# Kernel tuning notes

Measured on AMD Instinct MI355X. Metric: run time of the kernel, lower is better.

The kernel has to match this reference:

```python
import jax, jax.numpy as jnp
import numpy as np

HEADS = 16
HEAD_DIM = 64
DIM = 1024
INNER = HEADS * HEAD_DIM
EPS = 1e-5


def setup_inputs() -> dict:
    key = jax.random.key(0)
    k_x, k_qkv, k_out, k_b = jax.random.split(key, 4)
    B, L = 2, 2048
    x = jax.random.normal(k_x, (B, L, DIM), dtype=jnp.float32)
    # Linear weights stored as [in, out] for x @ W
    w_qkv = jax.random.normal(k_qkv, (DIM, 3 * INNER), dtype=jnp.float32) * (DIM ** -0.5)
    w_out = jax.random.normal(k_out, (INNER, DIM), dtype=jnp.float32) * (INNER ** -0.5)
    b_out = jax.random.normal(k_b, (DIM,), dtype=jnp.float32) * 0.02
    gamma = jnp.ones((DIM,), dtype=jnp.float32)
    beta = jnp.zeros((DIM,), dtype=jnp.float32)
    return {"x": x, "w_qkv": w_qkv, "w_out": w_out, "b_out": b_out, "gamma": gamma, "beta": beta}


def reference(x, w_qkv, w_out, b_out, gamma, beta):
    B, L, C = x.shape
    scale = HEAD_DIM ** -0.5
    qkv = x @ w_qkv  # [B, L, 3*INNER]
    q, k, v = jnp.split(qkv, 3, axis=-1)
    # [B, L, INNER] -> [B, H, L, D]
    def split_heads(t):
        return t.reshape(B, L, HEADS, HEAD_DIM).transpose(0, 2, 1, 3)
    q, k, v = split_heads(q), split_heads(k), split_heads(v)
    dots = jnp.einsum('bhid,bhjd->bhij', q, k) * scale
    attn = jax.nn.softmax(dots, axis=-1)
    out = jnp.einsum('bhij,bhjd->bhid', attn, v)
    out = out.transpose(0, 2, 1, 3).reshape(B, L, INNER)
    out = out @ w_out + b_out
    res = x + out
    mean = jnp.mean(res, axis=-1, keepdims=True)
    var = jnp.var(res, axis=-1, keepdims=True)
    return (res - mean) * jax.lax.rsqrt(var + EPS) * gamma + beta
```

## Files before the change

### kernel.cpp

```cpp
#include <hip/hip_runtime.h>
#include <hip/hip_bf16.h>
#include <stdint.h>

#define HEADS 16
#define HDIM  64
#define DIMC  1024
#define INNER 1024
#define LSEQ  2048
#define BLM   4096

typedef unsigned short u16;
typedef __attribute__((ext_vector_type(8))) short bf16x8;
typedef __attribute__((ext_vector_type(4))) float f32x4;

__device__ __forceinline__ u16 f2bf(float f) {
  union { float f; uint32_t u; } v; v.f = f;
  uint32_t u = v.u;
  return (u16)((u + 0x7fffu + ((u >> 16) & 1u)) >> 16);
}
__device__ __forceinline__ uint32_t pack_bf2(float a, float b) {
  float2 f2; f2.x = a; f2.y = b;
  __hip_bfloat162 t = __float22bfloat162_rn(f2);
  union { __hip_bfloat162 h; uint32_t u; } c; c.h = t; return c.u;
}
__device__ __forceinline__ float fast_exp2(float x) {
  float r; asm("v_exp_f32 %0, %1" : "=v"(r) : "v"(x)); return r;
}

__device__ __forceinline__ void load_lds16(const void* g, void* l) {
  __builtin_amdgcn_global_load_lds(
      (const __attribute__((address_space(1))) uint32_t*)g,
      (__attribute__((address_space(3))) uint32_t*)l, 16, 0, 0);
}

__global__ __launch_bounds__(256) void cast_bf16_k(const float* __restrict__ in,
                                                   u16* __restrict__ out, int n) {
  int i = (blockIdx.x * 256 + threadIdx.x) * 4;
  if (i < n) {
    float4 v = *(const float4*)(in + i);
    ushort4 o;
    o.x = f2bf(v.x); o.y = f2bf(v.y); o.z = f2bf(v.z); o.w = f2bf(v.w);
    *(ushort4*)(out + i) = o;
  }
}

__global__ __launch_bounds__(256) void transpose_cast_k(const float* __restrict__ in,
                                                        u16* __restrict__ out,
                                                        int R, int C) {
  __shared__ float tile[32][33];
  int c0 = blockIdx.x * 32, r0 = blockIdx.y * 32;
  int j = threadIdx.x & 31, i0 = threadIdx.x >> 5;
#pragma unroll
  for (int p = 0; p < 4; ++p) {
    int i = i0 + p * 8;
    tile[i][j] = in[(size_t)(r0 + i) * C + (c0 + j)];
  }
  __syncthreads();
#pragma unroll
  for (int p = 0; p < 4; ++p) {
    int i = i0 + p * 8;
    out[(size_t)(c0 + i) * R + (r0 + j)] = f2bf(tile[j][i]);
  }
}

template <int EPI, int TM>
__global__ __launch_bounds__(256) void gemm_bt(const u16* __restrict__ A,
                                               const u16* __restrict__ Bt,
                                               u16* __restrict__ Cb,
                                               float* __restrict__ Cf,
                                               const float* __restrict__ bias,
                                               const float* __restrict__ resid,
                                               u16* __restrict__ Vt,
                                               int M, int N, int K) {
  constexpr int MI = TM / 32;
  __shared__ alignas(16) u16 As[TM * 64];
  __shared__ alignas(16) u16 Bs[128 * 64];
  const int tid = threadIdx.x;
  const int lane = tid & 63;
  const int w = tid >> 6;
  const int wm = w >> 1, wn = w & 1;
  const int m0 = blockIdx.y * TM, n0 = blockIdx.x * 128;
  const int ln = lane & 15, qq = lane >> 4;
  const f32x4 zero4 = {0.f, 0.f, 0.f, 0.f};

  f32x4 acc[MI][4];
#pragma unroll
  for (int i = 0; i < MI; ++i)
#pragma unroll
    for (int j = 0; j < 4; ++j) acc[i][j] = zero4;

  for (int kt = 0; kt < K; kt += 64) {
    __syncthreads();
#pragma unroll
    for (int p = 0; p < TM / 32; ++p) {
      int t = p * 256 + tid;
      int r = t >> 3;
      int cl = (t & 7) ^ (r & 7);
      load_lds16(A + (size_t)(m0 + r) * K + kt + cl * 8,
                 (char*)As + (p * 256 + w * 64) * 16);
    }
#pragma unroll
    for (int p = 0; p < 4; ++p) {
      int t = p * 256 + tid;
      int r = t >> 3;
      int cl = (t & 7) ^ (r & 7);
      load_lds16(Bt + (size_t)(n0 + r) * K + kt + cl * 8,
                 (char*)Bs + (p * 256 + w * 64) * 16);
    }
    __syncthreads();
#pragma unroll
    for (int ks = 0; ks < 2; ++ks) {
      bf16x8 af[MI], bfr[4];
#pragma unroll
      for (int i = 0; i < MI; ++i) {
        int ra = wm * (TM / 2) + i * 16 + ln;
        af[i] = *(const bf16x8*)(As + (ra * 8 + ((ks * 4 + qq) ^ (ra & 7))) * 8);
      }
#pragma unroll
      for (int j = 0; j < 4; ++j) {
        int rb = wn * 64 + j * 16 + ln;
        bfr[j] = *(const bf16x8*)(Bs + (rb * 8 + ((ks * 4 + qq) ^ (rb & 7))) * 8);
      }
#pragma unroll
      for (int i = 0; i < MI; ++i)
#pragma unroll
        for (int j = 0; j < 4; ++j)
          acc[i][j] = __builtin_amdgcn_mfma_f32_16x16x32_bf16(af[i], bfr[j],
                                                              acc[i][j], 0, 0, 0);
    }
  }

#pragma unroll
  for (int i = 0; i < MI; ++i) {
#pragma unroll
    for (int j = 0; j < 4; ++j) {
      int col = n0 + wn * 64 + j * 16 + ln;
      if (EPI == 1) {
#pragma unroll
        for (int rr = 0; rr < 4; ++rr) {
          int row = m0 + wm * (TM / 2) + i * 16 + qq * 4 + rr;
          Cf[(size_t)row * N + col] =
              acc[i][j][rr] + bias[col] + resid[(size_t)row * N + col];
        }
      } else {
        if (col < 2048) {
#pragma unroll
          for (int rr = 0; rr < 4; ++rr) {
            int row = m0 + wm * (TM / 2) + i * 16 + qq * 4 + rr;
            Cb[(size_t)row * 2048 + col] = f2bf(acc[i][j][rr]);
          }
        } else {
          int dg = col - 2048;
          int hh = dg >> 6, dd = dg & 63;
          int l0 = (m0 & 2047) + wm * (TM / 2) + i * 16 + qq * 4;
          int bb = m0 >> 11;
          ushort4 pk;
          pk.x = f2bf(acc[i][j][0]); pk.y = f2bf(acc[i][j][1]);
          pk.z = f2bf(acc[i][j][2]); pk.w = f2bf(acc[i][j][3]);
          *(ushort4*)(Vt + (((size_t)bb * 16 + hh) * 64 + dd) * 2048 + l0) = pk;
        }
      }
    }
  }
}

__global__ __launch_bounds__(256) void attn_fused(const u16* __restrict__ qk,
                                                  const u16* __restrict__ vt,
                                                  u16* __restrict__ outp) {
  const int bh = blockIdx.x & 31;
  const int qt = blockIdx.x >> 5;
  const int h = bh & 15;
  const int b = bh >> 4;
  const int tid = threadIdx.x;
  const int lane = tid & 63;
  const int w = tid >> 6;
  const int ln = lane & 15, q4 = lane >> 4;
  const int l7 = ln & 7;
  const f32x4 zero4 = {0.f, 0.f, 0.f, 0.f};

  __shared__ alignas(16) u16 Ks[64 * 64];
  __shared__ alignas(16) u16 Vs[64 * 64];
  __shared__ alignas(16) u16 Ps[4][16 * 72];

  const size_t bh_tok = (size_t)b * LSEQ;
  const size_t vbase = ((size_t)b * 16 + h) * 64 * 2048;
  const int baseQ = h * HDIM;

  const float qscale = 0.125f * 1.44269504088896340736f;
  bf16x8 qf[2];
  {
    int row = qt * 64 + w * 16 + ln;
    const u16* p = qk + (bh_tok + row) * 2048 + baseQ;
#pragma unroll
    for (int ks = 0; ks < 2; ++ks) {
      bf16x8 v = *(const bf16x8*)(p + q4 * 8 + 32 * ks);
      bf16x8 o;
#pragma unroll
      for (int jj = 0; jj < 8; ++jj) {
        union { uint32_t u; float f; } cv; cv.u = ((uint32_t)(u16)v[jj]) << 16;
        o[jj] = (short)f2bf(cv.f * qscale);
      }
      qf[ks] = o;
    }
  }

  float lsum = 0.f;
  f32x4 o_acc[4];
#pragma unroll
  for (int dt = 0; dt < 4; ++dt) o_acc[dt] = zero4;

  u16* pw_base = &Ps[w][0];

  for (int jt = 0; jt < 32; ++jt) {
    const int key0 = jt * 64;
    __syncthreads();
#pragma unroll
    for (int iss = 0; iss < 2; ++iss) {
      int idx = iss * 256 + tid;
      int row = idx >> 3, c = idx & 7;
      int cl = c ^ (row & 7);
      load_lds16(qk + (bh_tok + key0 + row) * 2048 + 1024 + baseQ + cl * 8,
                 (char*)Ks + (iss * 256 + w * 64) * 16);
      load_lds16(vt + vbase + (size_t)row * 2048 + key0 + cl * 8,
                 (char*)Vs + (iss * 256 + w * 64) * 16);
    }
    __syncthreads();

    f32x4 S[4];
#pragma unroll
    for (int kt = 0; kt < 4; ++kt) {
      f32x4 a = zero4;
#pragma unroll
      for (int ks = 0; ks < 2; ++ks) {
        bf16x8 kf = *(const bf16x8*)(
            Ks + (((kt * 16 + ln) * 8 + ((ks * 4 + q4) ^ l7)) * 8));
        a = __builtin_amdgcn_mfma_f32_16x16x32_bf16(kf, qf[ks], a, 0, 0, 0);
      }
      S[kt] = a;
    }

#pragma unroll
    for (int kt = 0; kt < 4; ++kt)
#pragma unroll
      for (int r = 0; r < 4; ++r) {
        float p = fast_exp2(S[kt][r]);
        S[kt][r] = p;
        lsum += p;
      }

#pragma unroll
    for (int kt = 0; kt < 4; ++kt) {
      uint2 pd;
      pd.x = pack_bf2(S[kt][0], S[kt][1]);
      pd.y = pack_bf2(S[kt][2], S[kt][3]);
      *(uint2*)(pw_base + ln * 72 + kt * 16 + q4 * 4) = pd;
    }
    asm volatile("s_waitcnt lgkmcnt(0)" ::: "memory");

    bf16x8 pf0 = *(const bf16x8*)(pw_base + ln * 72 + 0 * 32 + q4 * 8);
    bf16x8 pf1 = *(const bf16x8*)(pw_base + ln * 72 + 1 * 32 + q4 * 8);

#pragma unroll
    for (int dt = 0; dt < 4; ++dt) {
      bf16x8 va0 = *(const bf16x8*)(
          Vs + (((dt * 16 + ln) * 8 + ((0 * 4 + q4) ^ l7)) * 8));
      o_acc[dt] = __builtin_amdgcn_mfma_f32_16x16x32_bf16(va0, pf0, o_acc[dt], 0, 0, 0);
      bf16x8 va1 = *(const bf16x8*)(
          Vs + (((dt * 16 + ln) * 8 + ((1 * 4 + q4) ^ l7)) * 8));
      o_acc[dt] = __builtin_amdgcn_mfma_f32_16x16x32_bf16(va1, pf1, o_acc[dt], 0, 0, 0);
    }
  }

  lsum += __shfl_xor(lsum, 16);
  lsum += __shfl_xor(lsum, 32);
  float rl = 1.0f / lsum;

  asm volatile("s_waitcnt lgkmcnt(0)" ::: "memory");
#pragma unroll
  for (int dt = 0; dt < 4; ++dt) {
    uint2 pd;
    pd.x = pack_bf2(o_acc[dt][0] * rl, o_acc[dt][1] * rl);
    pd.y = pack_bf2(o_acc[dt][2] * rl, o_acc[dt][3] * rl);
    *(uint2*)(pw_base + ln * 72 + dt * 16 + q4 * 4) = pd;
  }
  asm volatile("s_waitcnt lgkmcnt(0)" ::: "memory");
#pragma unroll
  for (int half = 0; half < 2; ++half) {
    int rr = half * 8 + (lane >> 3);
    int ch = lane & 7;
    bf16x8 rowv = *(const bf16x8*)(pw_base + rr * 72 + ch * 8);
    int tok = qt * 64 + w * 16 + rr;
    *(bf16x8*)(outp + (bh_tok + tok) * 1024 + baseQ + ch * 8) = rowv;
  }
}

__global__ __launch_bounds__(256) void ln_k(const float* __restrict__ res,
                                            const float* __restrict__ gamma,
                                            const float* __restrict__ beta,
                                            float* __restrict__ out) {
  int w = threadIdx.x >> 6, lane = threadIdx.x & 63;
  int row = blockIdx.x * 4 + w;
  const float* r = res + (size_t)row * DIMC;
  float4 v[4];
  float s = 0.f, ss = 0.f;
#pragma unroll
  for (int p = 0; p < 4; ++p) {
    v[p] = *(const float4*)(r + (p * 64 + lane) * 4);
    s += v[p].x + v[p].y + v[p].z + v[p].w;
    ss += v[p].x * v[p].x + v[p].y * v[p].y + v[p].z * v[p].z + v[p].w * v[p].w;
  }
#pragma unroll
  for (int off = 1; off < 64; off <<= 1) {
    s += __shfl_xor(s, off);
    ss += __shfl_xor(ss, off);
  }
  float mean = s * (1.0f / DIMC);
  float var = ss * (1.0f / DIMC) - mean * mean;
  float inv = rsqrtf(var + 1e-5f);
#pragma unroll
  for (int p = 0; p < 4; ++p) {
    int c = (p * 64 + lane) * 4;
    float4 g = *(const float4*)(gamma + c);
    float4 bt = *(const float4*)(beta + c);
    float4 o;
    o.x = (v[p].x - mean) * inv * g.x + bt.x;
    o.y = (v[p].y - mean) * inv * g.y + bt.y;
    o.z = (v[p].z - mean) * inv * g.z + bt.z;
    o.w = (v[p].w - mean) * inv * g.w + bt.w;
    *(float4*)(out + (size_t)row * DIMC + c) = o;
  }
}

extern "C" void kernel_launch(void* const* d_in, const int* in_sizes, int n_in,
                              void* d_out, int out_size, void* d_ws, size_t ws_size,
                              hipStream_t stream) {
  const float* x = (const float*)d_in[0];
  const float* w_qkv = (const float*)d_in[1];
  const float* w_out = (const float*)d_in[2];
  const float* b_out = (const float*)d_in[3];
  const float* gamma = (const float*)d_in[4];
  const float* beta = (const float*)d_in[5];
  float* outp = (float*)d_out;
  char* ws = (char*)d_ws;

  u16* xb = (u16*)(ws);
  u16* wqkvT = (u16*)(ws + ((size_t)8 << 20));
  u16* qk = (u16*)(ws + ((size_t)14 << 20));
  u16* vt = (u16*)(ws + ((size_t)30 << 20));
  u16* attnout = (u16*)(ws);
  u16* woutT = (u16*)(ws + ((size_t)8 << 20));
  float* res = (float*)(ws + ((size_t)14 << 20));

  cast_bf16_k<<<4096, 256, 0, stream>>>(x, xb, BLM * DIMC);
  transpose_cast_k<<<dim3(96, 32), 256, 0, stream>>>(w_qkv, wqkvT, 1024, 3072);
  gemm_bt<2, 128><<<dim3(24, 32), 256, 0, stream>>>(xb, wqkvT, qk, nullptr,
                                                    nullptr, nullptr, vt,
                                                    BLM, 3072, 1024);
  transpose_cast_k<<<dim3(32, 32), 256, 0, stream>>>(w_out, woutT, 1024, 1024);
  attn_fused<<<1024, 256, 0, stream>>>(qk, vt, attnout);
  gemm_bt<1, 64><<<dim3(8, 64), 256, 0, stream>>>(attnout, woutT, nullptr, res,
                                                  b_out, x, nullptr,
                                                  BLM, 1024, 1024);
  ln_k<<<1024, 256, 0, stream>>>(res, gamma, beta, outp);
}
```

Baseline: 209.5 us.

## Merge input cast and weight transpose into one prep kernel; XOR-swizzle P tile

Combines the x bf16 cast and the w_qkv transpose-cast into a single launch, using the block index to choose which job each block does, so one kernel launch and its gap go away. Separately, the per-wave P/output staging buffer in attention drops its padded row stride in favor of an XOR swizzle on 16-byte chunks, which shrinks LDS use and is meant to avoid bank conflicts on the bf16x8 reads. The swizzle adds index arithmetic, and the shared-memory tile is now declared in blocks that only do the plain cast.

```diff
diff --git a/kernel.cpp b/kernel.cpp
--- a/kernel.cpp
+++ b/kernel.cpp
@@ -33,14 +33,34 @@
       (__attribute__((address_space(3))) uint32_t*)l, 16, 0, 0);
 }
 
-__global__ __launch_bounds__(256) void cast_bf16_k(const float* __restrict__ in,
-                                                   u16* __restrict__ out, int n) {
-  int i = (blockIdx.x * 256 + threadIdx.x) * 4;
-  if (i < n) {
-    float4 v = *(const float4*)(in + i);
+__global__ __launch_bounds__(256) void prep_k(const float* __restrict__ x,
+                                              const float* __restrict__ w_qkv,
+                                              u16* __restrict__ xb,
+                                              u16* __restrict__ wqkvT) {
+  __shared__ float tile[32][33];
+  int bid = blockIdx.x;
+  if (bid < 4096) {
+    int i = (bid * 256 + threadIdx.x) * 4;
+    float4 v = *(const float4*)(x + i);
     ushort4 o;
     o.x = f2bf(v.x); o.y = f2bf(v.y); o.z = f2bf(v.z); o.w = f2bf(v.w);
-    *(ushort4*)(out + i) = o;
+    *(ushort4*)(xb + i) = o;
+    return;
+  }
+  int idx = bid - 4096;
+  int bx = idx % 96, by = idx / 96;
+  int c0 = bx * 32, r0 = by * 32;
+  int j = threadIdx.x & 31, i0 = threadIdx.x >> 5;
+#pragma unroll
+  for (int p = 0; p < 4; ++p) {
+    int i = i0 + p * 8;
+    tile[i][j] = w_qkv[(size_t)(r0 + i) * 3072 + (c0 + j)];
+  }
+  __syncthreads();
+#pragma unroll
+  for (int p = 0; p < 4; ++p) {
+    int i = i0 + p * 8;
+    wqkvT[(size_t)(c0 + i) * 1024 + (r0 + j)] = f2bf(tile[j][i]);
   }
 }
 
@@ -180,7 +200,7 @@
 
   __shared__ alignas(16) u16 Ks[64 * 64];
   __shared__ alignas(16) u16 Vs[64 * 64];
-  __shared__ alignas(16) u16 Ps[4][16 * 72];
+  __shared__ alignas(16) u16 Ps[4][16 * 64];
 
   const size_t bh_tok = (size_t)b * LSEQ;
   const size_t vbase = ((size_t)b * 16 + h) * 64 * 2048;
@@ -253,12 +273,13 @@
       uint2 pd;
       pd.x = pack_bf2(S[kt][0], S[kt][1]);
       pd.y = pack_bf2(S[kt][2], S[kt][3]);
-      *(uint2*)(pw_base + ln * 72 + kt * 16 + q4 * 4) = pd;
+      int u = kt * 2 + (q4 >> 1);
+      *(uint2*)(pw_base + ln * 64 + ((u ^ l7) * 8) + (q4 & 1) * 4) = pd;
     }
     asm volatile("s_waitcnt lgkmcnt(0)" ::: "memory");
 
-    bf16x8 pf0 = *(const bf16x8*)(pw_base + ln * 72 + 0 * 32 + q4 * 8);
-    bf16x8 pf1 = *(const bf16x8*)(pw_base + ln * 72 + 1 * 32 + q4 * 8);
+    bf16x8 pf0 = *(const bf16x8*)(pw_base + ln * 64 + (((0 * 4 + q4) ^ l7) * 8));
+    bf16x8 pf1 = *(const bf16x8*)(pw_base + ln * 64 + (((1 * 4 + q4) ^ l7) * 8));
 
 #pragma unroll
     for (int dt = 0; dt < 4; ++dt) {
@@ -281,14 +302,15 @@
     uint2 pd;
     pd.x = pack_bf2(o_acc[dt][0] * rl, o_acc[dt][1] * rl);
     pd.y = pack_bf2(o_acc[dt][2] * rl, o_acc[dt][3] * rl);
-    *(uint2*)(pw_base + ln * 72 + dt * 16 + q4 * 4) = pd;
+    int u = dt * 2 + (q4 >> 1);
+    *(uint2*)(pw_base + ln * 64 + ((u ^ l7) * 8) + (q4 & 1) * 4) = pd;
   }
   asm volatile("s_waitcnt lgkmcnt(0)" ::: "memory");
 #pragma unroll
   for (int half = 0; half < 2; ++half) {
     int rr = half * 8 + (lane >> 3);
     int ch = lane & 7;
-    bf16x8 rowv = *(const bf16x8*)(pw_base + rr * 72 + ch * 8);
+    bf16x8 rowv = *(const bf16x8*)(pw_base + rr * 64 + ((ch ^ (rr & 7)) * 8));
     int tok = qt * 64 + w * 16 + rr;
     *(bf16x8*)(outp + (bh_tok + tok) * 1024 + baseQ + ch * 8) = rowv;
   }
@@ -351,8 +373,7 @@
   u16* woutT = (u16*)(ws + ((size_t)8 << 20));
   float* res = (float*)(ws + ((size_t)14 << 20));
 
-  cast_bf16_k<<<4096, 256, 0, stream>>>(x, xb, BLM * DIMC);
-  transpose_cast_k<<<dim3(96, 32), 256, 0, stream>>>(w_qkv, wqkvT, 1024, 3072);
+  prep_k<<<7168, 256, 0, stream>>>(x, w_qkv, xb, wqkvT);
   gemm_bt<2, 128><<<dim3(24, 32), 256, 0, stream>>>(xb, wqkvT, qk, nullptr,
                                                     nullptr, nullptr, vt,
                                                     BLM, 3072, 1024);
```

Measured after the change: 203.6 us. 2.8% less time.
